# Kernel optimization log

Hardware: AMD Instinct MI355X
Metric: run time of the kernel (lower is better)

The kernel has to match this reference:

```python
import jax, jax.numpy as jnp
import numpy as np

N_NODES = 100000
N_EDGES = 6400000


def _gcn_conv(x, src, dst, W, b, num_nodes):
    # GCNConv: x' = D^{-1/2} (A + I) D^{-1/2} X W + b
    # (src/dst already include self-loops; deg computed on A+I at dst, PyG default flow)
    h = x @ W  # [N, out]
    ones = jnp.ones(src.shape[0], dtype=h.dtype)
    deg = jax.ops.segment_sum(ones, dst, num_segments=num_nodes)  # in-degree incl. self-loops
    dinv = jnp.where(deg > 0, deg ** -0.5, 0.0)  # [N]
    norm = dinv[src] * dinv[dst]  # [E]
    msg = h[src] * norm[:, None]  # gather + scale, [E, out]
    agg = jax.ops.segment_sum(msg, dst, num_segments=num_nodes)  # scatter-add, [N, out]
    return agg + b


def setup_inputs() -> dict:
    key = jax.random.key(0)
    k1, k2, k3, k4 = jax.random.split(key, 4)
    x = jax.random.normal(k1, (N_NODES, 1), dtype=jnp.float32)
    edge_index = jax.random.randint(k2, (2, N_EDGES), 0, N_NODES, dtype=jnp.int64)
    # Glorot-style init for GCN weights
    W1 = jax.random.normal(k3, (1, 16), dtype=jnp.float32) * (2.0 / (1 + 16)) ** 0.5
    b1 = jnp.zeros((16,), dtype=jnp.float32)
    W2 = jax.random.normal(k4, (16, 2), dtype=jnp.float32) * (2.0 / (16 + 2)) ** 0.5
    b2 = jnp.zeros((2,), dtype=jnp.float32)
    return {"x": x, "edge_index": edge_index, "W1": W1, "b1": b1, "W2": W2, "b2": b2}


def reference(x, edge_index, W1, b1, W2, b2):
    num_nodes = x.shape[0]
    loops = jnp.arange(num_nodes, dtype=edge_index.dtype)
    src = jnp.concatenate([edge_index[0], loops])
    dst = jnp.concatenate([edge_index[1], loops])
    h = jax.nn.relu(_gcn_conv(x, src, dst, W1, b1, num_nodes))
    # F.dropout with training=False (eval) is identity
    out = _gcn_conv(h, src, dst, W2, b2, num_nodes)
    return jax.nn.log_softmax(out, axis=1)
```

## Files before the change

### kernel.cpp

```cpp
#include <hip/hip_runtime.h>
#include <hip/hip_fp16.h>

#define TPB 256
#define LOG_NPB 9
#define NPB 512
#define SPLIT 16
#define CHUNK 4096
#define EPT 16
#define KMAX 256


__device__ __forceinline__ void lds_pk_add_f16(unsigned* addr, unsigned val) {
  asm volatile("ds_pk_add_f16 %0, %1"
               :: "v"((unsigned)(unsigned long long)addr), "v"(val)
               : "memory");
}

__global__ void k_reset(int* __restrict__ gcur, int K) {
  int i = blockIdx.x * blockDim.x + threadIdx.x;
  if (i < K) gcur[i] = 0;
}

__global__ __launch_bounds__(TPB) void
k_bucket(const int* __restrict__ src, const int* __restrict__ dst,
         int E, int K, int cap,
         int* __restrict__ gcur, unsigned int* __restrict__ packed) {
  __shared__ unsigned int stage[CHUNK];
  __shared__ unsigned char bkt[CHUNK];
  __shared__ int hist[KMAX], start[KMAX], cur[KMAX], res[KMAX];
  __shared__ int sc[KMAX];

  const int t = threadIdx.x;
  const int e0 = blockIdx.x * CHUNK;
  const int e1 = min(e0 + CHUNK, E);
  const int cn = e1 - e0;

  for (int b = t; b < KMAX; b += TPB) hist[b] = 0;
  __syncthreads();

  unsigned int pk[EPT];
  unsigned int bb4[EPT / 4];
#pragma unroll
  for (int q = 0; q < EPT / 4; ++q) bb4[q] = 0xFFFFFFFFu;

#pragma unroll
  for (int q = 0; q < EPT / 4; ++q) {
    int base = e0 + 4 * t + q * 4 * TPB;
    if (base + 4 <= e1) {
      int4 dv = *reinterpret_cast<const int4*>(dst + base);
      int4 sv = *reinterpret_cast<const int4*>(src + base);
      int d[4] = {dv.x, dv.y, dv.z, dv.w};
      int s[4] = {sv.x, sv.y, sv.z, sv.w};
#pragma unroll
      for (int j = 0; j < 4; ++j) {
        int b = d[j] >> LOG_NPB;
        pk[4 * q + j] = ((unsigned)s[j] << LOG_NPB) | (unsigned)(d[j] & (NPB - 1));
        bb4[q] = (bb4[q] & ~(0xFFu << (8 * j))) | ((unsigned)b << (8 * j));
        atomicAdd(&hist[b], 1);
      }
    } else {
      for (int j = 0; j < 4; ++j) {
        int idx = base + j;
        if (idx < e1) {
          int d = dst[idx], s = src[idx];
          int b = d >> LOG_NPB;
          pk[4 * q + j] = ((unsigned)s << LOG_NPB) | (unsigned)(d & (NPB - 1));
          bb4[q] = (bb4[q] & ~(0xFFu << (8 * j))) | ((unsigned)b << (8 * j));
          atomicAdd(&hist[b], 1);
        }
      }
    }
  }
  __syncthreads();

  int hv = hist[t];
  sc[t] = hv;
  __syncthreads();
#pragma unroll
  for (int off = 1; off < KMAX; off <<= 1) {
    int u = (t >= off) ? sc[t - off] : 0;
    __syncthreads();
    sc[t] += u;
    __syncthreads();
  }
  start[t] = sc[t] - hv;
  cur[t] = sc[t] - hv;
  res[t] = (t < K && hv > 0) ? atomicAdd(&gcur[t], hv) : 0;
  __syncthreads();

#pragma unroll
  for (int k = 0; k < EPT; ++k) {
    int b = (bb4[k >> 2] >> (8 * (k & 3))) & 255;
    if (b != 255) {
      int p = atomicAdd(&cur[b], 1);
      stage[p] = pk[k];
      bkt[p] = (unsigned char)b;
    }
  }
  __syncthreads();

  for (int i = t; i < cn; i += TPB) {
    int b = bkt[i];
    int gp = res[b] + i - start[b];
    if (gp < cap) packed[(size_t)b * cap + gp] = stage[i];
  }
}

__device__ __forceinline__ void slice_range(int cnt, int s, int& off0, int& off1) {
  off0 = (int)(((long long)cnt * s) / SPLIT) & ~3;
  off1 = (s == SPLIT - 1) ? cnt : (int)(((long long)cnt * (s + 1)) / SPLIT) & ~3;
}

__global__ __launch_bounds__(TPB) void
k_deg(const unsigned int* __restrict__ packed, const int* __restrict__ gcur,
      int cap, int* __restrict__ pdeg, int Npad) {
  int b = blockIdx.x / SPLIT, s = blockIdx.x % SPLIT;
  __shared__ int bins[NPB];
  for (int i = threadIdx.x; i < NPB; i += TPB) bins[i] = 0;
  __syncthreads();
  int cnt = min(gcur[b], cap);
  int off0, off1; slice_range(cnt, s, off0, off1);
  const unsigned int* base = packed + (size_t)b * cap;
  int len = off1 - off0;
  int nfull = len >> 3;
  for (int g = threadIdx.x; g < nfull; g += TPB) {
    int e = off0 + (g << 3);
    uint4 pa = *reinterpret_cast<const uint4*>(base + e);
    uint4 pb = *reinterpret_cast<const uint4*>(base + e + 4);
    atomicAdd(&bins[pa.x & (NPB - 1)], 1);
    atomicAdd(&bins[pa.y & (NPB - 1)], 1);
    atomicAdd(&bins[pa.z & (NPB - 1)], 1);
    atomicAdd(&bins[pa.w & (NPB - 1)], 1);
    atomicAdd(&bins[pb.x & (NPB - 1)], 1);
    atomicAdd(&bins[pb.y & (NPB - 1)], 1);
    atomicAdd(&bins[pb.z & (NPB - 1)], 1);
    atomicAdd(&bins[pb.w & (NPB - 1)], 1);
  }
  for (int e = off0 + (nfull << 3) + threadIdx.x; e < off1; e += TPB)
    atomicAdd(&bins[base[e] & (NPB - 1)], 1);
  __syncthreads();
  int nb = b << LOG_NPB;
  for (int i = threadIdx.x; i < NPB; i += TPB)
    pdeg[s * Npad + nb + i] = bins[i];
}

__global__ void k_dinv(const int* __restrict__ pdeg, const float* __restrict__ x,
                       float* __restrict__ dinv, float* __restrict__ xd,
                       int N, int Npad) {
  int i = blockIdx.x * TPB + threadIdx.x;
  if (i >= N) return;
  int d = 1;
#pragma unroll
  for (int s = 0; s < SPLIT; ++s) d += pdeg[s * Npad + i];
  float di = rsqrtf((float)d);
  dinv[i] = di;
  xd[i] = x[i] * di;
}

__global__ __launch_bounds__(TPB) void
k_pass1(const unsigned int* __restrict__ packed, const int* __restrict__ gcur,
        int cap, const float* __restrict__ xd, float* __restrict__ pt1, int Npad) {
  int b = blockIdx.x / SPLIT, s = blockIdx.x % SPLIT;
  __shared__ float bins[NPB];
  for (int i = threadIdx.x; i < NPB; i += TPB) bins[i] = 0.f;
  __syncthreads();
  int cnt = min(gcur[b], cap);
  int off0, off1; slice_range(cnt, s, off0, off1);
  const unsigned int* base = packed + (size_t)b * cap;
  int len = off1 - off0;
  int nfull = len >> 3;
  for (int g = threadIdx.x; g < nfull; g += TPB) {
    int e = off0 + (g << 3);
    uint4 pa = *reinterpret_cast<const uint4*>(base + e);
    uint4 pb = *reinterpret_cast<const uint4*>(base + e + 4);
    float v0 = xd[pa.x >> LOG_NPB];
    float v1 = xd[pa.y >> LOG_NPB];
    float v2 = xd[pa.z >> LOG_NPB];
    float v3 = xd[pa.w >> LOG_NPB];
    float v4 = xd[pb.x >> LOG_NPB];
    float v5 = xd[pb.y >> LOG_NPB];
    float v6 = xd[pb.z >> LOG_NPB];
    float v7 = xd[pb.w >> LOG_NPB];
    atomicAdd(&bins[pa.x & (NPB - 1)], v0);
    atomicAdd(&bins[pa.y & (NPB - 1)], v1);
    atomicAdd(&bins[pa.z & (NPB - 1)], v2);
    atomicAdd(&bins[pa.w & (NPB - 1)], v3);
    atomicAdd(&bins[pb.x & (NPB - 1)], v4);
    atomicAdd(&bins[pb.y & (NPB - 1)], v5);
    atomicAdd(&bins[pb.z & (NPB - 1)], v6);
    atomicAdd(&bins[pb.w & (NPB - 1)], v7);
  }
  for (int e = off0 + (nfull << 3) + threadIdx.x; e < off1; e += TPB) {
    unsigned int p = base[e];
    atomicAdd(&bins[p & (NPB - 1)], xd[p >> LOG_NPB]);
  }
  __syncthreads();
  int nb = b << LOG_NPB;
  for (int i = threadIdx.x; i < NPB; i += TPB)
    pt1[s * Npad + nb + i] = bins[i];
}

__global__ void k_node(const float* __restrict__ pt1, const float* __restrict__ xd,
                       const float* __restrict__ dinv,
                       const float* __restrict__ W1, const float* __restrict__ b1,
                       const float* __restrict__ W2,
                       unsigned* __restrict__ gdp, int N, int Npad) {
  int i = blockIdx.x * TPB + threadIdx.x;
  if (i >= N) return;
  float tv = 0.f;
#pragma unroll
  for (int s = 0; s < SPLIT; ++s) tv += pt1[s * Npad + i];
  float di = dinv[i];
  float sv = di * (tv + xd[i]);
  float g0 = 0.f, g1 = 0.f;
#pragma unroll
  for (int j = 0; j < 16; ++j) {
    float h = fmaxf(fmaf(sv, W1[j], b1[j]), 0.f);
    g0 = fmaf(h, W2[2 * j], g0);
    g1 = fmaf(h, W2[2 * j + 1], g1);
  }
  __half2 h2 = __floats2half2_rn(g0 * di, g1 * di);
  gdp[i] = *reinterpret_cast<unsigned*>(&h2);
}

__global__ __launch_bounds__(TPB) void
k_pass2(const unsigned int* __restrict__ packed, const int* __restrict__ gcur,
        int cap, const unsigned* __restrict__ gdp, float* __restrict__ pt2, int Npad) {
  int b = blockIdx.x / SPLIT, s = blockIdx.x % SPLIT;
  __shared__ unsigned bins[NPB];
  for (int i = threadIdx.x; i < NPB; i += TPB) bins[i] = 0u;
  __syncthreads();
  int cnt = min(gcur[b], cap);
  int off0, off1; slice_range(cnt, s, off0, off1);
  const unsigned int* base = packed + (size_t)b * cap;
  int len = off1 - off0;
  int nfull = len >> 3;
  for (int g = threadIdx.x; g < nfull; g += TPB) {
    int e = off0 + (g << 3);
    uint4 pa = *reinterpret_cast<const uint4*>(base + e);
    uint4 pb = *reinterpret_cast<const uint4*>(base + e + 4);
    unsigned v0 = gdp[pa.x >> LOG_NPB];
    unsigned v1 = gdp[pa.y >> LOG_NPB];
    unsigned v2 = gdp[pa.z >> LOG_NPB];
    unsigned v3 = gdp[pa.w >> LOG_NPB];
    unsigned v4 = gdp[pb.x >> LOG_NPB];
    unsigned v5 = gdp[pb.y >> LOG_NPB];
    unsigned v6 = gdp[pb.z >> LOG_NPB];
    unsigned v7 = gdp[pb.w >> LOG_NPB];
    lds_pk_add_f16(&bins[pa.x & (NPB - 1)], v0);
    lds_pk_add_f16(&bins[pa.y & (NPB - 1)], v1);
    lds_pk_add_f16(&bins[pa.z & (NPB - 1)], v2);
    lds_pk_add_f16(&bins[pa.w & (NPB - 1)], v3);
    lds_pk_add_f16(&bins[pb.x & (NPB - 1)], v4);
    lds_pk_add_f16(&bins[pb.y & (NPB - 1)], v5);
    lds_pk_add_f16(&bins[pb.z & (NPB - 1)], v6);
    lds_pk_add_f16(&bins[pb.w & (NPB - 1)], v7);
  }
  for (int e = off0 + (nfull << 3) + threadIdx.x; e < off1; e += TPB) {
    unsigned int p = base[e];
    lds_pk_add_f16(&bins[p & (NPB - 1)], gdp[p >> LOG_NPB]);
  }
  __syncthreads();
  int nb = b << LOG_NPB;
  for (int i = threadIdx.x; i < NPB; i += TPB) {
    __half2 h = *reinterpret_cast<__half2*>(&bins[i]);
    float2 o;
    o.x = __low2float(h);
    o.y = __high2float(h);
    *reinterpret_cast<float2*>(pt2 + (size_t)s * 2 * Npad + 2 * (nb + i)) = o;
  }
}

__global__ void k_final(const float* __restrict__ pt2, const unsigned* __restrict__ gdp,
                        const float* __restrict__ dinv, const float* __restrict__ b2,
                        float* __restrict__ out, int N, int Npad) {
  int i = blockIdx.x * TPB + threadIdx.x;
  if (i >= N) return;
  float t0 = 0.f, t1 = 0.f;
#pragma unroll
  for (int s = 0; s < SPLIT; ++s) {
    float2 p = *reinterpret_cast<const float2*>(pt2 + (size_t)s * 2 * Npad + 2 * i);
    t0 += p.x;
    t1 += p.y;
  }
  unsigned gp = gdp[i];
  __half2 h = *reinterpret_cast<__half2*>(&gp);
  float di = dinv[i];
  float o0 = di * (t0 + __low2float(h)) + b2[0];
  float o1 = di * (t1 + __high2float(h)) + b2[1];
  float m = fmaxf(o0, o1);
  float l = m + logf(expf(o0 - m) + expf(o1 - m));
  out[2 * i] = o0 - l;
  out[2 * i + 1] = o1 - l;
}

extern "C" void kernel_launch(void* const* d_in, const int* in_sizes, int n_in,
                              void* d_out, int out_size, void* d_ws, size_t ws_size,
                              hipStream_t stream) {
  const float* x  = (const float*)d_in[0];
  const int*   ei = (const int*)d_in[1];
  const float* W1 = (const float*)d_in[2];
  const float* b1 = (const float*)d_in[3];
  const float* W2 = (const float*)d_in[4];
  const float* b2 = (const float*)d_in[5];

  const int N = in_sizes[0];
  const int E = in_sizes[1] / 2;
  const int* src = ei;
  const int* dst = ei + E;

  const int K = (N + NPB - 1) >> LOG_NPB;
  const int Npad = K << LOG_NPB;
  int mean = (int)(((long long)E * NPB) / N);
  int cap = mean + mean / 16 + 512;
  cap = (cap + 3) & ~3;

  char* ws = (char*)d_ws;
  auto align256 = [&](size_t n) { char* p = ws; ws += (n + 255) & ~(size_t)255; return p; };

  int*          gcur   = (int*)align256((size_t)K * 4);
  unsigned int* packed = (unsigned int*)align256((size_t)K * cap * 4);
  float*        dinv   = (float*)align256((size_t)N * 4);
  float*        xd     = (float*)align256((size_t)N * 4);
  unsigned*     gdp    = (unsigned*)align256((size_t)N * 4);
  float*        R      = (float*)align256((size_t)SPLIT * 2 * Npad * 4);
  int*          pdeg   = (int*)R;
  float*        pt1    = R;
  float*        pt2    = R;

  float* out = (float*)d_out;

  int nb_node   = (N + TPB - 1) / TPB;
  int nb_bucket = (E + CHUNK - 1) / CHUNK;
  int nb_acc    = K * SPLIT;

  k_reset <<<(K + TPB - 1) / TPB, TPB, 0, stream>>>(gcur, K);
  k_bucket<<<nb_bucket, TPB, 0, stream>>>(src, dst, E, K, cap, gcur, packed);
  k_deg   <<<nb_acc, TPB, 0, stream>>>(packed, gcur, cap, pdeg, Npad);
  k_dinv  <<<nb_node, TPB, 0, stream>>>(pdeg, x, dinv, xd, N, Npad);
  k_pass1 <<<nb_acc, TPB, 0, stream>>>(packed, gcur, cap, xd, pt1, Npad);
  k_node  <<<nb_node, TPB, 0, stream>>>(pt1, xd, dinv, W1, b1, W2, gdp, N, Npad);
  k_pass2 <<<nb_acc, TPB, 0, stream>>>(packed, gcur, cap, gdp, pt2, Npad);
  k_final <<<nb_node, TPB, 0, stream>>>(pt2, gdp, dinv, b2, out, N, Npad);
}
```

Baseline: 153.6 us.

## Replace histogram-scan bucketing with fixed-capacity per-bucket LDS slots and global overflow

The bucketing kernel no longer builds a per-block histogram and prefix scan before staging. Each edge now claims a slot in a fixed-size per-bucket LDS region, and any edge past that capacity is written directly to global memory through a global atomic. This removes the scan's many barriers and the register staging of edges. In exchange it adds uncoalesced global atomics and writes for overflowing buckets, and the flush loop runs over every slot including empty ones.

Result: faster. 147.6 us (-3.9%).

```diff
diff --git a/kernel.cpp b/kernel.cpp
--- a/kernel.cpp
+++ b/kernel.cpp
@@ -6,8 +6,7 @@
 #define NPB 512
 #define SPLIT 16
 #define CHUNK 4096
-#define EPT 16
-#define KMAX 256
+#define RCAP 44
 
 
 __device__ __forceinline__ void lds_pk_add_f16(unsigned* addr, unsigned val) {
@@ -23,29 +22,21 @@
 
 __global__ __launch_bounds__(TPB) void
 k_bucket(const int* __restrict__ src, const int* __restrict__ dst,
-         int E, int K, int cap,
+         int E, int K, int capG,
          int* __restrict__ gcur, unsigned int* __restrict__ packed) {
-  __shared__ unsigned int stage[CHUNK];
-  __shared__ unsigned char bkt[CHUNK];
-  __shared__ int hist[KMAX], start[KMAX], cur[KMAX], res[KMAX];
-  __shared__ int sc[KMAX];
+  extern __shared__ unsigned smem[];
+  unsigned* stage = smem;
+  int* cur = (int*)(smem + (size_t)K * RCAP);
+  int* res = cur + K;
 
   const int t = threadIdx.x;
   const int e0 = blockIdx.x * CHUNK;
   const int e1 = min(e0 + CHUNK, E);
-  const int cn = e1 - e0;
-
-  for (int b = t; b < KMAX; b += TPB) hist[b] = 0;
-  __syncthreads();
-
-  unsigned int pk[EPT];
-  unsigned int bb4[EPT / 4];
-#pragma unroll
-  for (int q = 0; q < EPT / 4; ++q) bb4[q] = 0xFFFFFFFFu;
-
-#pragma unroll
-  for (int q = 0; q < EPT / 4; ++q) {
-    int base = e0 + 4 * t + q * 4 * TPB;
+
+  for (int b = t; b < K; b += TPB) cur[b] = 0;
+  __syncthreads();
+
+  for (int base = e0 + 4 * t; base < e1; base += 4 * TPB) {
     if (base + 4 <= e1) {
       int4 dv = *reinterpret_cast<const int4*>(dst + base);
       int4 sv = *reinterpret_cast<const int4*>(src + base);
@@ -54,9 +45,14 @@
 #pragma unroll
       for (int j = 0; j < 4; ++j) {
         int b = d[j] >> LOG_NPB;
-        pk[4 * q + j] = ((unsigned)s[j] << LOG_NPB) | (unsigned)(d[j] & (NPB - 1));
-        bb4[q] = (bb4[q] & ~(0xFFu << (8 * j))) | ((unsigned)b << (8 * j));
-        atomicAdd(&hist[b], 1);
+        unsigned pk = ((unsigned)s[j] << LOG_NPB) | (unsigned)(d[j] & (NPB - 1));
+        int p = atomicAdd(&cur[b], 1);
+        if (p < RCAP) {
+          stage[b * RCAP + p] = pk;
+        } else {
+          int gp = atomicAdd(&gcur[b], 1);
+          if (gp < capG) packed[(size_t)b * capG + gp] = pk;
+        }
       }
     } else {
       for (int j = 0; j < 4; ++j) {
@@ -64,45 +60,34 @@
         if (idx < e1) {
           int d = dst[idx], s = src[idx];
           int b = d >> LOG_NPB;
-          pk[4 * q + j] = ((unsigned)s << LOG_NPB) | (unsigned)(d & (NPB - 1));
-          bb4[q] = (bb4[q] & ~(0xFFu << (8 * j))) | ((unsigned)b << (8 * j));
-          atomicAdd(&hist[b], 1);
+          unsigned pk = ((unsigned)s << LOG_NPB) | (unsigned)(d & (NPB - 1));
+          int p = atomicAdd(&cur[b], 1);
+          if (p < RCAP) {
+            stage[b * RCAP + p] = pk;
+          } else {
+            int gp = atomicAdd(&gcur[b], 1);
+            if (gp < capG) packed[(size_t)b * capG + gp] = pk;
+          }
         }
       }
     }
   }
   __syncthreads();
 
-  int hv = hist[t];
-  sc[t] = hv;
-  __syncthreads();
-#pragma unroll
-  for (int off = 1; off < KMAX; off <<= 1) {
-    int u = (t >= off) ? sc[t - off] : 0;
-    __syncthreads();
-    sc[t] += u;
-    __syncthreads();
-  }
-  start[t] = sc[t] - hv;
-  cur[t] = sc[t] - hv;
-  res[t] = (t < K && hv > 0) ? atomicAdd(&gcur[t], hv) : 0;
-  __syncthreads();
-
-#pragma unroll
-  for (int k = 0; k < EPT; ++k) {
-    int b = (bb4[k >> 2] >> (8 * (k & 3))) & 255;
-    if (b != 255) {
-      int p = atomicAdd(&cur[b], 1);
-      stage[p] = pk[k];
-      bkt[p] = (unsigned char)b;
+  if (t < K) {
+    int c = min(cur[t], RCAP);
+    res[t] = (c > 0) ? atomicAdd(&gcur[t], c) : 0;
+  }
+  __syncthreads();
+
+  const int tot = K * RCAP;
+  for (int i = t; i < tot; i += TPB) {
+    int b = i / RCAP;
+    int pos = i - b * RCAP;
+    if (pos < min(cur[b], RCAP)) {
+      int gp = res[b] + pos;
+      if (gp < capG) packed[(size_t)b * capG + gp] = stage[i];
     }
-  }
-  __syncthreads();
-
-  for (int i = t; i < cn; i += TPB) {
-    int b = bkt[i];
-    int gp = res[b] + i - start[b];
-    if (gp < cap) packed[(size_t)b * cap + gp] = stage[i];
   }
 }
 
@@ -333,9 +318,10 @@
   int nb_node   = (N + TPB - 1) / TPB;
   int nb_bucket = (E + CHUNK - 1) / CHUNK;
   int nb_acc    = K * SPLIT;
+  size_t sh_bucket = ((size_t)K * RCAP + 2 * (size_t)K) * 4;
 
   k_reset <<<(K + TPB - 1) / TPB, TPB, 0, stream>>>(gcur, K);
-  k_bucket<<<nb_bucket, TPB, 0, stream>>>(src, dst, E, K, cap, gcur, packed);
+  k_bucket<<<nb_bucket, TPB, sh_bucket, stream>>>(src, dst, E, K, cap, gcur, packed);
   k_deg   <<<nb_acc, TPB, 0, stream>>>(packed, gcur, cap, pdeg, Npad);
   k_dinv  <<<nb_node, TPB, 0, stream>>>(pdeg, x, dinv, xd, N, Npad);
   k_pass1 <<<nb_acc, TPB, 0, stream>>>(packed, gcur, cap, xd, pt1, Npad);
```
